# Kernel tuning notes

Measured on AMD Instinct MI355X. Metric: run time of the kernel, lower is better.

The kernel has to match this reference:

```python
import jax, jax.numpy as jnp
import numpy as np

N_NODES = 100000
N_EDGES = 600000
IN_DIM = 128
HID = 128


def setup_inputs() -> dict:
    key = jax.random.key(0)
    ks = jax.random.split(key, 9)
    x = jax.random.normal(ks[0], (N_NODES, IN_DIM), dtype=jnp.float32)
    edge_index = jax.random.randint(ks[1], (2, N_EDGES), 0, N_NODES, dtype=jnp.int64)
    s = 1.0 / np.sqrt(IN_DIM)
    # PyG SAGEConv: out = lin_l(mean_aggr(x_src)) + lin_r(x_root); lin_l carries the bias.
    W_l0 = jax.random.uniform(ks[2], (IN_DIM, HID), jnp.float32, -s, s)
    b_l0 = jnp.zeros((HID,), jnp.float32)
    W_r0 = jax.random.uniform(ks[3], (IN_DIM, HID), jnp.float32, -s, s)
    s2 = 1.0 / np.sqrt(HID)
    W_l1 = jax.random.uniform(ks[4], (HID, HID), jnp.float32, -s2, s2)
    b_l1 = jnp.zeros((HID,), jnp.float32)
    W_r1 = jax.random.uniform(ks[5], (HID, HID), jnp.float32, -s2, s2)
    return {"x": x, "edge_index": edge_index,
            "W_l0": W_l0, "b_l0": b_l0, "W_r0": W_r0,
            "W_l1": W_l1, "b_l1": b_l1, "W_r1": W_r1}


def _sage_mean_conv(h, src, dst, W_l, b_l, W_r):
    # gather source-node features per edge, scatter-mean into destinations
    msgs = h[src]                                              # [E, D]
    sums = jax.ops.segment_sum(msgs, dst, num_segments=N_NODES)  # [N, D]
    cnt = jax.ops.segment_sum(jnp.ones((src.shape[0],), h.dtype), dst,
                              num_segments=N_NODES)             # [N]
    mean = sums / jnp.maximum(cnt, 1.0)[:, None]
    return mean @ W_l + b_l + h @ W_r


def reference(x, edge_index, W_l0, b_l0, W_r0, W_l1, b_l1, W_r1):
    src, dst = edge_index[0], edge_index[1]
    h = _sage_mean_conv(x, src, dst, W_l0, b_l0, W_r0)
    h = jax.nn.relu(h)  # dropout is identity in eval mode
    h = _sage_mean_conv(h, src, dst, W_l1, b_l1, W_r1)
    h = jax.nn.relu(h)
    return h
```

## Files before the change

### kernel.cpp

```cpp
#include <hip/hip_runtime.h>

#define N_NODES 100000
#define N_EDGES 600000
#define DIM 128

typedef __attribute__((ext_vector_type(8))) short bf16x8;
typedef __attribute__((ext_vector_type(4))) float f32x4;

typedef __attribute__((address_space(1))) const unsigned int g_u32;
typedef __attribute__((address_space(3))) unsigned int l_u32;
__device__ __forceinline__ void stage16(const void* g, void* l) {
  __builtin_amdgcn_global_load_lds((g_u32*)g, (l_u32*)l, 16, 0, 0);
}

__device__ __forceinline__ unsigned short f32_to_bf16_rn(float f) {
  unsigned int u = __builtin_bit_cast(unsigned int, f);
  unsigned int r = (u + 0x7FFFu + ((u >> 16) & 1u)) >> 16;
  return (unsigned short)r;
}
__device__ __forceinline__ float bf16_to_f32(unsigned short h) {
  return __builtin_bit_cast(float, (unsigned int)h << 16);
}

__global__ __launch_bounds__(256) void xsplit_k(const float* __restrict__ in,
                                                unsigned short* __restrict__ hi) {
  const int i = blockIdx.x * 256 + threadIdx.x;
  const float4 v = reinterpret_cast<const float4*>(in)[i];
  const float f[4] = {v.x, v.y, v.z, v.w};
  unsigned short h[4];
#pragma unroll
  for (int j = 0; j < 4; ++j) h[j] = f32_to_bf16_rn(f[j]);
  uint2 hp;
  hp.x = (unsigned)h[0] | ((unsigned)h[1] << 16);
  hp.y = (unsigned)h[2] | ((unsigned)h[3] << 16);
  reinterpret_cast<uint2*>(hi)[i] = hp;
}

__global__ __launch_bounds__(256) void pack_w_k(
    const float* __restrict__ Wl0, const float* __restrict__ Wr0,
    const float* __restrict__ Wl1, const float* __restrict__ Wr1,
    unsigned short* __restrict__ P0, unsigned short* __restrict__ P1) {
  const int gid = blockIdx.x * 256 + threadIdx.x;
  const int layer = gid >> 15;
  const int idx = gid & 32767;
  const int j = idx & 7;
  const int l = (idx >> 3) & 63;
  const int nt = (idx >> 9) & 7;
  const int g = idx >> 12;
  const int k = ((g & 3) << 5) + ((l >> 4) << 3) + j;
  const int n = (nt << 4) + (l & 15);
  const float* W = layer ? ((g < 4) ? Wl1 : Wr1) : ((g < 4) ? Wl0 : Wr0);
  (layer ? P1 : P0)[idx] = f32_to_bf16_rn(W[k * 128 + n]);
}

__global__ void hist_k(const int* __restrict__ dst, int* __restrict__ deg) {
  int e = blockIdx.x * blockDim.x + threadIdx.x;
  if (e < N_EDGES) atomicAdd(&deg[dst[e]], 1);
}

__global__ __launch_bounds__(1024) void scan1_k(const int* __restrict__ deg,
                                                int* __restrict__ incl,
                                                int* __restrict__ bsum) {
  __shared__ int wsum[16];
  const int t = threadIdx.x, lane = t & 63, w = t >> 6;
  const int gi = blockIdx.x * 1024 + t;
  int v = (gi < N_NODES) ? deg[gi] : 0;
  int s = v;
#pragma unroll
  for (int off = 1; off < 64; off <<= 1) {
    int u = __shfl_up(s, off);
    if (lane >= off) s += u;
  }
  if (lane == 63) wsum[w] = s;
  __syncthreads();
  if (t < 16) {
    int ws = wsum[t];
#pragma unroll
    for (int off = 1; off < 16; off <<= 1) {
      int u = __shfl_up(ws, off);
      if (t >= off) ws += u;
    }
    wsum[t] = ws;
  }
  __syncthreads();
  const int val = s + (w ? wsum[w - 1] : 0);
  if (gi < N_NODES) incl[gi] = val;
  if (t == 1023) bsum[blockIdx.x] = val;
}

__global__ void scan2_k(const int* __restrict__ bsum, int* __restrict__ boffs,
                        int nb) {
  __shared__ int w0;
  const int t = threadIdx.x;
  int v = (t < nb) ? bsum[t] : 0;
  int s = v;
#pragma unroll
  for (int off = 1; off < 64; off <<= 1) {
    int u = __shfl_up(s, off);
    if ((t & 63) >= off) s += u;
  }
  if (t == 63) w0 = s;
  __syncthreads();
  const int excl = s - v + ((t >> 6) ? w0 : 0);
  if (t < nb) boffs[t] = excl;
}

__global__ __launch_bounds__(1024) void scan3_k(const int* __restrict__ deg,
                                                const int* __restrict__ incl,
                                                const int* __restrict__ boffs,
                                                int* __restrict__ rowptr,
                                                int* __restrict__ head) {
  const int gi = blockIdx.x * 1024 + threadIdx.x;
  if (gi < N_NODES) {
    const int e = incl[gi] - deg[gi] + boffs[blockIdx.x];
    rowptr[gi] = e;
    head[gi] = e;
  }
  if (gi == 0) rowptr[N_NODES] = N_EDGES;
}

__global__ void fill_k(const int* __restrict__ src, const int* __restrict__ dst,
                       int* __restrict__ head, int* __restrict__ col) {
  int e = blockIdx.x * blockDim.x + threadIdx.x;
  if (e < N_EDGES) {
    int p = atomicAdd(&head[dst[e]], 1);
    col[p] = src[e];
  }
}

__global__ __launch_bounds__(256) void agg_k(
    const unsigned short* __restrict__ plane, const int* __restrict__ rowptr,
    const int* __restrict__ col, unsigned short* __restrict__ mhi) {
  const int t = threadIdx.x;
  const int node = blockIdx.x * 16 + (t >> 4);
  const int q = t & 15;
  const int beg = rowptr[node], end = rowptr[node + 1];
  const uint4* P = reinterpret_cast<const uint4*>(plane);
  float a[8] = {};

  auto accum = [&](uint4 v) {
    const unsigned int u[4] = {v.x, v.y, v.z, v.w};
#pragma unroll
    for (int w = 0; w < 4; ++w) {
      a[2 * w] += __builtin_bit_cast(float, u[w] << 16);
      a[2 * w + 1] += __builtin_bit_cast(float, u[w] & 0xFFFF0000u);
    }
  };

  for (int i = beg; i < end; i += 4) {
    const int i1 = min(i + 1, end - 1);
    const int i2 = min(i + 2, end - 1);
    const int i3 = min(i + 3, end - 1);
    const int c0 = col[i], c1 = col[i1], c2 = col[i2], c3 = col[i3];
    const uint4 v0 = P[(size_t)c0 * 16 + q];
    const uint4 v1 = P[(size_t)c1 * 16 + q];
    const uint4 v2 = P[(size_t)c2 * 16 + q];
    const uint4 v3 = P[(size_t)c3 * 16 + q];
    accum(v0);
    if (i + 1 < end) accum(v1);
    if (i + 2 < end) accum(v2);
    if (i + 3 < end) accum(v3);
  }

  const int d = end - beg;
  const float inv = 1.0f / (float)(d > 1 ? d : 1);
  unsigned int hw[4];
#pragma unroll
  for (int w = 0; w < 4; ++w) {
    const unsigned short h0 = f32_to_bf16_rn(a[2 * w] * inv);
    const unsigned short h1 = f32_to_bf16_rn(a[2 * w + 1] * inv);
    hw[w] = (unsigned)h0 | ((unsigned)h1 << 16);
  }
  uint4 ho = {hw[0], hw[1], hw[2], hw[3]};
  reinterpret_cast<uint4*>(mhi)[(size_t)node * 16 + q] = ho;
}

template <int OUTF32>
__global__ __launch_bounds__(256, 4) void gemm_k(
    const unsigned short* __restrict__ Mhi, const unsigned short* __restrict__ Hhi,
    const unsigned short* __restrict__ Bp, const float* __restrict__ bias,
    unsigned short* __restrict__ Ohi, float* __restrict__ Of) {
  __shared__ unsigned short Bl[2][4096];
  const int t = threadIdx.x;
  const int lane = t & 63;
  const int wid = t >> 6;
  const int rbase = blockIdx.x * 64 + wid * 16;
  const int lm = lane & 15, lk = lane >> 4;
  const size_t r0 = (size_t)min(rbase + lm, N_NODES - 1);

  f32x4 acc[8] = {};

  auto stageG = [&](int g, int nb) {
#pragma unroll
    for (int c = 0; c < 2; ++c) {
      const int e = (c * 256 + t) * 8;
      stage16(Bp + (size_t)g * 4096 + e, &Bl[nb][e]);
    }
  };
  auto loadA = [&](int g) {
    const unsigned short* P = (g < 4) ? Mhi : Hhi;
    const int ke = ((g & 3) << 5) + (lk << 3);
    return *reinterpret_cast<const bf16x8*>(P + r0 * DIM + ke);
  };

  stageG(0, 0);
  bf16x8 ca = loadA(0), na;
  __syncthreads();

#pragma unroll
  for (int g = 0; g < 8; ++g) {
    const int buf = g & 1;
    if (g < 7) {
      stageG(g + 1, buf ^ 1);
      na = loadA(g + 1);
    }
#pragma unroll
    for (int nt = 0; nt < 8; ++nt) {
      const bf16x8 b =
          *reinterpret_cast<const bf16x8*>(&Bl[buf][(nt * 64 + lane) * 8]);
      acc[nt] = __builtin_amdgcn_mfma_f32_16x16x32_bf16(ca, b, acc[nt], 0, 0, 0);
    }
    __syncthreads();
    ca = na;
  }

#pragma unroll
  for (int nt = 0; nt < 8; ++nt) {
    const int cidx = nt * 16 + lm;
    const float bv = bias[cidx];
#pragma unroll
    for (int i = 0; i < 4; ++i) {
      const int r = rbase + lk * 4 + i;
      if (r < N_NODES) {
        float v = acc[nt][i] + bv;
        v = fmaxf(v, 0.0f);
        if (OUTF32) {
          Of[(size_t)r * DIM + cidx] = v;
        } else {
          Ohi[(size_t)r * DIM + cidx] = f32_to_bf16_rn(v);
        }
      }
    }
  }
}

extern "C" void kernel_launch(void* const* d_in, const int* in_sizes, int n_in,
                              void* d_out, int out_size, void* d_ws,
                              size_t ws_size, hipStream_t stream) {
  const float* x = (const float*)d_in[0];
  const int* ei = (const int*)d_in[1];
  const float* Wl0 = (const float*)d_in[2];
  const float* bl0 = (const float*)d_in[3];
  const float* Wr0 = (const float*)d_in[4];
  const float* Wl1 = (const float*)d_in[5];
  const float* bl1 = (const float*)d_in[6];
  const float* Wr1 = (const float*)d_in[7];
  float* out = (float*)d_out;
  const int* src = ei;
  const int* dst = ei + N_EDGES;

  char* p = (char*)d_ws;
  auto alloc = [&](size_t bytes) {
    char* q = p;
    p += (bytes + 255) & ~(size_t)255;
    return q;
  };
  int* deg = (int*)alloc((size_t)N_NODES * 4);
  int* rowptr = (int*)alloc((size_t)(N_NODES + 1) * 4);
  int* head = (int*)alloc((size_t)N_NODES * 4);
  int* col = (int*)alloc((size_t)N_EDGES * 4);
  int* bsum = (int*)alloc(128 * 4);
  int* boffs = (int*)alloc(128 * 4);
  unsigned short* Bp0 = (unsigned short*)alloc(32768 * 2);
  unsigned short* Bp1 = (unsigned short*)alloc(32768 * 2);
  unsigned short* xhi = (unsigned short*)alloc((size_t)N_NODES * DIM * 2);
  unsigned short* mhi = (unsigned short*)alloc((size_t)N_NODES * DIM * 2);
  unsigned short* h1hi = (unsigned short*)alloc((size_t)N_NODES * DIM * 2);

  const int nScanB = (N_NODES + 1023) / 1024;

  hipMemsetAsync(deg, 0, (size_t)N_NODES * 4, stream);
  pack_w_k<<<256, 256, 0, stream>>>(Wl0, Wr0, Wl1, Wr1, Bp0, Bp1);
  xsplit_k<<<(N_NODES * DIM / 4) / 256, 256, 0, stream>>>(x, xhi);
  hist_k<<<(N_EDGES + 255) / 256, 256, 0, stream>>>(dst, deg);
  scan1_k<<<nScanB, 1024, 0, stream>>>(deg, head, bsum);
  scan2_k<<<1, 128, 0, stream>>>(bsum, boffs, nScanB);
  scan3_k<<<nScanB, 1024, 0, stream>>>(deg, head, boffs, rowptr, head);
  fill_k<<<(N_EDGES + 255) / 256, 256, 0, stream>>>(src, dst, head, col);

  const int nBlocks = (N_NODES + 63) / 64;
  const int aggBlocks = N_NODES / 16;

  agg_k<<<aggBlocks, 256, 0, stream>>>(xhi, rowptr, col, mhi);
  gemm_k<0><<<nBlocks, 256, 0, stream>>>(mhi, xhi, Bp0, bl0, h1hi, nullptr);
  agg_k<<<aggBlocks, 256, 0, stream>>>(h1hi, rowptr, col, mhi);
  gemm_k<1><<<nBlocks, 256, 0, stream>>>(mhi, h1hi, Bp1, bl1, nullptr, out);
}
```

Baseline: 184.0 us.

## Double GEMM rows per wave and fuse weight-pack with x bf16 conversion

Each GEMM wave now computes two 16-row M tiles against the same staged B fragments, so every block covers 128 rows and each B tile read from LDS is reused twice. This halves the block count and the number of B stages. It also merges the weight-packing and x-to-bf16 kernels into one launch to save a kernel launch. The cost is more accumulator registers per thread, which may reduce occupancy under launch_bounds(256,4).

```diff
diff --git a/kernel.cpp b/kernel.cpp
--- a/kernel.cpp
+++ b/kernel.cpp
@@ -18,39 +18,38 @@
   unsigned int r = (u + 0x7FFFu + ((u >> 16) & 1u)) >> 16;
   return (unsigned short)r;
 }
-__device__ __forceinline__ float bf16_to_f32(unsigned short h) {
-  return __builtin_bit_cast(float, (unsigned int)h << 16);
-}
-
-__global__ __launch_bounds__(256) void xsplit_k(const float* __restrict__ in,
-                                                unsigned short* __restrict__ hi) {
-  const int i = blockIdx.x * 256 + threadIdx.x;
-  const float4 v = reinterpret_cast<const float4*>(in)[i];
-  const float f[4] = {v.x, v.y, v.z, v.w};
-  unsigned short h[4];
-#pragma unroll
-  for (int j = 0; j < 4; ++j) h[j] = f32_to_bf16_rn(f[j]);
-  uint2 hp;
-  hp.x = (unsigned)h[0] | ((unsigned)h[1] << 16);
-  hp.y = (unsigned)h[2] | ((unsigned)h[3] << 16);
-  reinterpret_cast<uint2*>(hi)[i] = hp;
-}
-
-__global__ __launch_bounds__(256) void pack_w_k(
+
+__global__ __launch_bounds__(256) void prep_k(
     const float* __restrict__ Wl0, const float* __restrict__ Wr0,
     const float* __restrict__ Wl1, const float* __restrict__ Wr1,
-    unsigned short* __restrict__ P0, unsigned short* __restrict__ P1) {
+    unsigned short* __restrict__ P0, unsigned short* __restrict__ P1,
+    const float* __restrict__ x, unsigned short* __restrict__ xhi) {
   const int gid = blockIdx.x * 256 + threadIdx.x;
-  const int layer = gid >> 15;
-  const int idx = gid & 32767;
-  const int j = idx & 7;
-  const int l = (idx >> 3) & 63;
-  const int nt = (idx >> 9) & 7;
-  const int g = idx >> 12;
-  const int k = ((g & 3) << 5) + ((l >> 4) << 3) + j;
-  const int n = (nt << 4) + (l & 15);
-  const float* W = layer ? ((g < 4) ? Wl1 : Wr1) : ((g < 4) ? Wl0 : Wr0);
-  (layer ? P1 : P0)[idx] = f32_to_bf16_rn(W[k * 128 + n]);
+  if (gid < 65536) {
+    const int layer = gid >> 15;
+    const int idx = gid & 32767;
+    const int j = idx & 7;
+    const int l = (idx >> 3) & 63;
+    const int nt = (idx >> 9) & 7;
+    const int g = idx >> 12;
+    const int k = ((g & 3) << 5) + ((l >> 4) << 3) + j;
+    const int n = (nt << 4) + (l & 15);
+    const float* W = layer ? ((g < 4) ? Wl1 : Wr1) : ((g < 4) ? Wl0 : Wr0);
+    (layer ? P1 : P0)[idx] = f32_to_bf16_rn(W[k * 128 + n]);
+  } else {
+    const int i = gid - 65536;
+    if (i < N_NODES * DIM / 4) {
+      const float4 v = reinterpret_cast<const float4*>(x)[i];
+      const float f[4] = {v.x, v.y, v.z, v.w};
+      unsigned short h[4];
+#pragma unroll
+      for (int j = 0; j < 4; ++j) h[j] = f32_to_bf16_rn(f[j]);
+      uint2 hp;
+      hp.x = (unsigned)h[0] | ((unsigned)h[1] << 16);
+      hp.y = (unsigned)h[2] | ((unsigned)h[3] << 16);
+      reinterpret_cast<uint2*>(xhi)[i] = hp;
+    }
+  }
 }
 
 __global__ void hist_k(const int* __restrict__ dst, int* __restrict__ deg) {
@@ -184,11 +183,12 @@
   const int t = threadIdx.x;
   const int lane = t & 63;
   const int wid = t >> 6;
-  const int rbase = blockIdx.x * 64 + wid * 16;
+  const int rbase = blockIdx.x * 128 + wid * 32;
   const int lm = lane & 15, lk = lane >> 4;
   const size_t r0 = (size_t)min(rbase + lm, N_NODES - 1);
-
-  f32x4 acc[8] = {};
+  const size_t r1 = (size_t)min(rbase + 16 + lm, N_NODES - 1);
+
+  f32x4 acc[2][8] = {};
 
   auto stageG = [&](int g, int nb) {
 #pragma unroll
@@ -197,14 +197,16 @@
       stage16(Bp + (size_t)g * 4096 + e, &Bl[nb][e]);
     }
   };
-  auto loadA = [&](int g) {
+  auto loadA = [&](int g, bf16x8& a0, bf16x8& a1) {
     const unsigned short* P = (g < 4) ? Mhi : Hhi;
     const int ke = ((g & 3) << 5) + (lk << 3);
-    return *reinterpret_cast<const bf16x8*>(P + r0 * DIM + ke);
+    a0 = *reinterpret_cast<const bf16x8*>(P + r0 * DIM + ke);
+    a1 = *reinterpret_cast<const bf16x8*>(P + r1 * DIM + ke);
   };
 
+  bf16x8 ca0, ca1, na0, na1;
   stageG(0, 0);
-  bf16x8 ca = loadA(0), na;
+  loadA(0, ca0, ca1);
   __syncthreads();
 
 #pragma unroll
@@ -212,16 +214,18 @@
     const int buf = g & 1;
     if (g < 7) {
       stageG(g + 1, buf ^ 1);
-      na = loadA(g + 1);
+      loadA(g + 1, na0, na1);
     }
 #pragma unroll
     for (int nt = 0; nt < 8; ++nt) {
       const bf16x8 b =
           *reinterpret_cast<const bf16x8*>(&Bl[buf][(nt * 64 + lane) * 8]);
-      acc[nt] = __builtin_amdgcn_mfma_f32_16x16x32_bf16(ca, b, acc[nt], 0, 0, 0);
+      acc[0][nt] = __builtin_amdgcn_mfma_f32_16x16x32_bf16(ca0, b, acc[0][nt], 0, 0, 0);
+      acc[1][nt] = __builtin_amdgcn_mfma_f32_16x16x32_bf16(ca1, b, acc[1][nt], 0, 0, 0);
     }
     __syncthreads();
-    ca = na;
+    ca0 = na0;
+    ca1 = na1;
   }
 
 #pragma unroll
@@ -229,15 +233,18 @@
     const int cidx = nt * 16 + lm;
     const float bv = bias[cidx];
 #pragma unroll
-    for (int i = 0; i < 4; ++i) {
-      const int r = rbase + lk * 4 + i;
-      if (r < N_NODES) {
-        float v = acc[nt][i] + bv;
-        v = fmaxf(v, 0.0f);
-        if (OUTF32) {
-          Of[(size_t)r * DIM + cidx] = v;
-        } else {
-          Ohi[(size_t)r * DIM + cidx] = f32_to_bf16_rn(v);
+    for (int mt = 0; mt < 2; ++mt) {
+#pragma unroll
+      for (int i = 0; i < 4; ++i) {
+        const int r = rbase + mt * 16 + lk * 4 + i;
+        if (r < N_NODES) {
+          float v = acc[mt][nt][i] + bv;
+          v = fmaxf(v, 0.0f);
+          if (OUTF32) {
+            Of[(size_t)r * DIM + cidx] = v;
+          } else {
+            Ohi[(size_t)r * DIM + cidx] = f32_to_bf16_rn(v);
+          }
         }
       }
     }
@@ -280,15 +287,15 @@
   const int nScanB = (N_NODES + 1023) / 1024;
 
   hipMemsetAsync(deg, 0, (size_t)N_NODES * 4, stream);
-  pack_w_k<<<256, 256, 0, stream>>>(Wl0, Wr0, Wl1, Wr1, Bp0, Bp1);
-  xsplit_k<<<(N_NODES * DIM / 4) / 256, 256, 0, stream>>>(x, xhi);
+  prep_k<<<(65536 + N_NODES * DIM / 4 + 255) / 256, 256, 0, stream>>>(
+      Wl0, Wr0, Wl1, Wr1, Bp0, Bp1, x, xhi);
   hist_k<<<(N_EDGES + 255) / 256, 256, 0, stream>>>(dst, deg);
   scan1_k<<<nScanB, 1024, 0, stream>>>(deg, head, bsum);
   scan2_k<<<1, 128, 0, stream>>>(bsum, boffs, nScanB);
   scan3_k<<<nScanB, 1024, 0, stream>>>(deg, head, boffs, rowptr, head);
   fill_k<<<(N_EDGES + 255) / 256, 256, 0, stream>>>(src, dst, head, col);
 
-  const int nBlocks = (N_NODES + 63) / 64;
+  const int nBlocks = (N_NODES + 127) / 128;
   const int aggBlocks = N_NODES / 16;
 
   agg_k<<<aggBlocks, 256, 0, stream>>>(xhi, rowptr, col, mhi);
```

Result: no change. 187.5 us (+1.9%).
